# Performance work log

Measured on AMD Instinct MI355X. Metric: run time of the kernel, lower is better.

The kernel has to match this reference:

```python
import jax, jax.numpy as jnp
import numpy as np

B, S, D = 2, 2048, 1024
H, DH = 16, 64  # n_heads, d_head = d_model // n_heads


def setup_inputs() -> dict:
    key = jax.random.key(0)
    ks = jax.random.split(key, 12)
    scale = 1.0 / np.sqrt(D)
    return {
        "queries": jax.random.normal(ks[0], (B, S, D), jnp.float32),
        "keys": jax.random.normal(ks[1], (B, S, D), jnp.float32),
        "values": jax.random.normal(ks[2], (B, S, D), jnp.float32),
        "mask": jax.random.randint(ks[3], (1, 1, S, S), 0, 2, jnp.int32),
        "Wq": jax.random.normal(ks[4], (D, D), jnp.float32) * scale,
        "bq": jnp.zeros((D,), jnp.float32),
        "Wk": jax.random.normal(ks[5], (D, D), jnp.float32) * scale,
        "bk": jnp.zeros((D,), jnp.float32),
        "Wv": jax.random.normal(ks[6], (D, D), jnp.float32) * scale,
        "bv": jnp.zeros((D,), jnp.float32),
        "Wo": jax.random.normal(ks[7], (D, D), jnp.float32) * scale,
        "bo": jnp.zeros((D,), jnp.float32),
    }


def _split_proj(x):
    # (B, ?, H, DH) reshape then permute -> (B, H, ?, DH)
    b = x.shape[0]
    return x.reshape(b, -1, H, DH).transpose(0, 2, 1, 3)


def reference(queries, keys, values, mask, Wq, bq, Wk, bk, Wv, bv, Wo, bo):
    q = queries @ Wq.T + bq
    k = keys @ Wk.T + bk
    v = values @ Wv.T + bv
    # NOTE: original source applies split_proj to queries twice (faithful repro)
    q = _split_proj(_split_proj(q))
    k = _split_proj(k)
    v = _split_proj(v)
    scores = jnp.einsum('bhqd,bhkd->bhqk', q, k) / jnp.sqrt(jnp.float32(DH))
    scores = scores + mask.astype(scores.dtype) * (-1e9)
    attn = jax.nn.softmax(scores, axis=-1)
    out = jnp.einsum('bhqk,bhkd->bhqd', attn, v)  # (B,H,S,DH)
    out = out.transpose(0, 2, 1, 3).reshape(out.shape[0], -1, D)
    return out @ Wo.T + bo
```

## Files before the change

### kernel.cpp

```cpp
#include <hip/hip_runtime.h>
#include <hip/hip_bf16.h>
#include <cstddef>
#include <cstdint>


typedef __attribute__((ext_vector_type(8))) short bf16x8;
typedef __attribute__((ext_vector_type(4))) float f32x4;

__device__ __forceinline__ void gl_lds16(const void* g, void* l) {
    __builtin_amdgcn_global_load_lds(
        (const __attribute__((address_space(1))) void*)g,
        (__attribute__((address_space(3))) void*)l, 16, 0, 0);
}

__device__ __forceinline__ int4 cvt8(const float* __restrict__ src) {
    const float4 v0 = *(const float4*)src, v1 = *(const float4*)(src + 4);
    union { __hip_bfloat16 h[8]; int4 q; } u;
    u.h[0] = __float2bfloat16(v0.x); u.h[1] = __float2bfloat16(v0.y);
    u.h[2] = __float2bfloat16(v0.z); u.h[3] = __float2bfloat16(v0.w);
    u.h[4] = __float2bfloat16(v1.x); u.h[5] = __float2bfloat16(v1.y);
    u.h[6] = __float2bfloat16(v1.z); u.h[7] = __float2bfloat16(v1.w);
    return u.q;
}

__global__ __launch_bounds__(256) void prep(
    const float* __restrict__ q, const float* __restrict__ k, const float* __restrict__ v,
    const float* __restrict__ wq, const float* __restrict__ wk,
    const float* __restrict__ wv, const float* __restrict__ wo,
    const int* __restrict__ mask,
    __hip_bfloat16* __restrict__ dq, __hip_bfloat16* __restrict__ dk,
    __hip_bfloat16* __restrict__ dv, __hip_bfloat16* __restrict__ dwq,
    __hip_bfloat16* __restrict__ dwk, __hip_bfloat16* __restrict__ dwv,
    __hip_bfloat16* __restrict__ dwo,
    unsigned long long* __restrict__ mbits)
{
    const int bid = blockIdx.x;
    if (bid >= 8192) {
        const int wid  = ((bid - 8192) * 256 + threadIdx.x) >> 6;
        const int lane = threadIdx.x & 63;
        const int qr = wid >> 5, w64 = wid & 31;
        const int m = mask[(size_t)qr * 2048 + w64 * 64 + lane];
        const unsigned long long bal = __ballot(m != 0);
        if (lane == 0) mbits[(size_t)qr * 32 + w64] = bal;
        return;
    }
    const float* s; __hip_bfloat16* d; int base;
    if      (bid < 2048) { s = q;  d = dq;  base = bid; }
    else if (bid < 4096) { s = k;  d = dk;  base = bid - 2048; }
    else if (bid < 6144) { s = v;  d = dv;  base = bid - 4096; }
    else if (bid < 6656) { s = wq; d = dwq; base = bid - 6144; }
    else if (bid < 7168) { s = wk; d = dwk; base = bid - 6656; }
    else if (bid < 7680) { s = wv; d = dwv; base = bid - 7168; }
    else                 { s = wo; d = dwo; base = bid - 7680; }
    const size_t i = (size_t)base * 256 + threadIdx.x;
    *((int4*)d + i) = cvt8(s + i * 8);
}

template <int MR, typename OutT>
__device__ __forceinline__ void gemm_body(
    const __hip_bfloat16* __restrict__ A, const __hip_bfloat16* __restrict__ Bm,
    const float* __restrict__ bias, OutT* __restrict__ C,
    int N, int m0, int n0, int brow,
    __hip_bfloat16* As, __hip_bfloat16* Bs)
{
    const int t = threadIdx.x, lane = t & 63, w = t >> 6;
    const int l15 = lane & 15, g = lane >> 4;
    const int wr = w >> 1, wc = w & 1;
    constexpr int NI = MR / 32;

    f32x4 acc[NI][4] = {};

    for (int k0 = 0; k0 < 1024; k0 += 64) {
        __syncthreads();
        #pragma unroll
        for (int it = 0; it < NI; ++it) {
            const int c = it * 256 + t, row = c >> 3, c8 = c & 7;
            gl_lds16(A + (size_t)(m0 + row) * 1024 + k0 + c8 * 8, (char*)As + c * 16);
        }
        #pragma unroll
        for (int it = 0; it < 4; ++it) {
            const int c = it * 256 + t, row = c >> 3, c8 = c & 7;
            gl_lds16(Bm + (size_t)(n0 + row) * 1024 + k0 + c8 * 8, (char*)Bs + c * 16);
        }
        __syncthreads();
        #pragma unroll
        for (int kk = 0; kk < 64; kk += 32) {
            bf16x8 af[NI], bfr[4];
            #pragma unroll
            for (int i = 0; i < NI; ++i)
                af[i] = *(const bf16x8*)((const char*)As + (wr * (MR / 2) + i * 16 + l15) * 128 + kk * 2 + g * 16);
            #pragma unroll
            for (int j = 0; j < 4; ++j)
                bfr[j] = *(const bf16x8*)((const char*)Bs + (wc * 64 + j * 16 + l15) * 128 + kk * 2 + g * 16);
            #pragma unroll
            for (int i = 0; i < NI; ++i)
                #pragma unroll
                for (int j = 0; j < 4; ++j)
                    acc[i][j] = __builtin_amdgcn_mfma_f32_16x16x32_bf16(af[i], bfr[j], acc[i][j], 0, 0, 0);
        }
    }

    #pragma unroll
    for (int i = 0; i < NI; ++i) {
        const int m = m0 + wr * (MR / 2) + i * 16 + g * 4;
        #pragma unroll
        for (int j = 0; j < 4; ++j) {
            const int n = n0 + wc * 64 + j * 16 + l15;
            const float bc = brow ? 0.f : bias[n];
            #pragma unroll
            for (int r = 0; r < 4; ++r) {
                const float v = acc[i][j][r] + (brow ? bias[m + r] : bc);
                C[(size_t)(m + r) * N + n] = (OutT)v;
            }
        }
    }
}

__global__ __launch_bounds__(256) void qkv_gemm(
    const __hip_bfloat16* __restrict__ qin, const __hip_bfloat16* __restrict__ kin,
    const __hip_bfloat16* __restrict__ vin,
    const __hip_bfloat16* __restrict__ Wqb, const __hip_bfloat16* __restrict__ Wkb,
    const __hip_bfloat16* __restrict__ Wvb,
    const float* __restrict__ bq, const float* __restrict__ bk, const float* __restrict__ bv,
    __hip_bfloat16* __restrict__ qbuf, __hip_bfloat16* __restrict__ kbuf,
    __hip_bfloat16* __restrict__ vtb)
{
    __shared__ __align__(16) __hip_bfloat16 As[128 * 64];
    __shared__ __align__(16) __hip_bfloat16 Bs[128 * 64];
    const int z = blockIdx.z;
    if (z == 0)
        gemm_body<128>(qin, Wqb, bq, qbuf, 1024, blockIdx.y * 128, blockIdx.x * 128, 0, As, Bs);
    else if (z == 1)
        gemm_body<128>(kin, Wkb, bk, kbuf, 1024, blockIdx.y * 128, blockIdx.x * 128, 0, As, Bs);
    else
        gemm_body<128>(Wvb, vin, bv, vtb, 4096, blockIdx.x * 128, blockIdx.y * 128, 1, As, Bs);
}

__global__ __launch_bounds__(256) void out_gemm(
    const __hip_bfloat16* __restrict__ A, const __hip_bfloat16* __restrict__ Bm,
    const float* __restrict__ bias, float* __restrict__ C)
{
    __shared__ __align__(16) __hip_bfloat16 As[64 * 64];
    __shared__ __align__(16) __hip_bfloat16 Bs[128 * 64];
    gemm_body<64>(A, Bm, bias, C, 1024, blockIdx.y * 64, blockIdx.x * 128, 0, As, Bs);
}

__global__ __launch_bounds__(512, 4) void attn_mfma(
    const __hip_bfloat16* __restrict__ qb,
    const __hip_bfloat16* __restrict__ kb,
    const __hip_bfloat16* __restrict__ vt,
    const unsigned long long* __restrict__ mbits,
    __hip_bfloat16* __restrict__ ctx)
{
    __shared__ __align__(16) char smem[65536];

    const int t = threadIdx.x, lane = t & 63, w = t >> 6;
    const int grp = w >> 2, wl = w & 3;
    const int l15 = lane & 15, g = lane >> 4;
    const int tloc = t & 255;

    const int bid = blockIdx.x;
    const int xcd = bid & 7, ii = bid >> 3;
    const int bh = (xcd << 2) + (ii >> 4), qt = ii & 15;
    const int b = bh >> 4, a = bh & 15;
    const int q0 = qt * 128;
    const int kt0 = grp * 16;

    constexpr float SC_LOG2E = 0.18033688011112042f;
    constexpr float OFFC     = -17.312340490667561f;
    constexpr float MASKB    = -1.0e9f;

    bf16x8 qreg[2][2];
    int qgl[2];
    #pragma unroll
    for (int u = 0; u < 2; ++u) {
        const int qg = q0 + wl * 32 + u * 16 + l15;
        qgl[u] = qg;
        const int srow = (qg & 127) * 16 + a;
        #pragma unroll
        for (int half = 0; half < 2; ++half)
            qreg[u][half] = *(const bf16x8*)&qb[(size_t)(b * 2048 + srow) * 1024 + qt * 64 + (half * 4 + g) * 8];
    }

    const int srow0 = tloc >> 3, scc = tloc & 7;
    const int scs = scc ^ (srow0 & 7);
    const char* kSrc = (const char*)(kb + (size_t)(b * 2048 + kt0 * 64 + srow0) * 1024 + a * 64 + scs * 8);
    const char* vSrc = (const char*)(vt + (size_t)(a * 64 + srow0) * 4096 + b * 2048 + kt0 * 64 + scs * 8);
    char* kDst = smem + grp * 16384 + tloc * 16;
    char* vDst = smem + 32768 + grp * 16384 + tloc * 16;

    auto stage = [&](int bufn) {
        gl_lds16(kSrc,          kDst + bufn * 8192);
        gl_lds16(kSrc + 65536,  kDst + bufn * 8192 + 4096);
        gl_lds16(vSrc,          vDst + bufn * 8192);
        gl_lds16(vSrc + 262144, vDst + bufn * 8192 + 4096);
        kSrc += 131072;
        vSrc += 128;
    };

    int kofs[2][4], vofs[2][4];
    #pragma unroll
    for (int x = 0; x < 2; ++x)
        #pragma unroll
        for (int nf = 0; nf < 4; ++nf) {
            const int rr = nf * 16 + l15;
            const int sw = ((x * 4 + g) ^ (rr & 7)) << 4;
            kofs[x][nf] = grp * 16384 + rr * 128 + sw;
            vofs[x][nf] = 32768 + grp * 16384 + rr * 128 + sw;
        }

    const unsigned long long* mbP0 = mbits + (size_t)qgl[0] * 32 + kt0;
    const unsigned long long* mbP1 = mbits + (size_t)qgl[1] * 32 + kt0;

    bf16x8 ones;
    #pragma unroll
    for (int e = 0; e < 8; ++e) ones[e] = (short)0x3F80;

    f32x4 accd[2][4] = {};
    f32x4 accl[2] = {};

    stage(0);
    __syncthreads();

    auto do_tile = [&](int buf, bool doStage) {
        if (doStage) stage(buf ^ 1);
        const uint2 mw0 = *(const uint2*)mbP0; ++mbP0;
        const uint2 mw1 = *(const uint2*)mbP1; ++mbP1;

        f32x4 sf[2][4] = {};
        #pragma unroll
        for (int half = 0; half < 2; ++half)
            #pragma unroll
            for (int nf = 0; nf < 4; ++nf) {
                const bf16x8 kf = *(const bf16x8*)(smem + kofs[half][nf] + buf * 8192);
                sf[0][nf] = __builtin_amdgcn_mfma_f32_16x16x32_bf16(kf, qreg[0][half], sf[0][nf], 0, 0, 0);
                sf[1][nf] = __builtin_amdgcn_mfma_f32_16x16x32_bf16(kf, qreg[1][half], sf[1][nf], 0, 0, 0);
            }

        unsigned Wrd[2][4][2];
        #pragma unroll
        for (int u = 0; u < 2; ++u) {
            const uint2 mwv = u ? mw1 : mw0;
            #pragma unroll
            for (int nf = 0; nf < 4; ++nf) {
                const unsigned word = (nf & 2) ? mwv.y : mwv.x;
                const int bsh = ((nf & 1) << 4) + (g << 2);
                float pr[4];
                #pragma unroll
                for (int r = 0; r < 4; ++r) {
                    const bool msk = (word >> (bsh + r)) & 1u;
                    pr[r] = __builtin_amdgcn_exp2f(
                        fmaf(sf[u][nf][r], SC_LOG2E, msk ? MASKB : OFFC));
                }
                Wrd[u][nf][0] = __builtin_amdgcn_perm(
                    __float_as_uint(pr[1]) + 0x8000u,
                    __float_as_uint(pr[0]) + 0x8000u, 0x07060302u);
                Wrd[u][nf][1] = __builtin_amdgcn_perm(
                    __float_as_uint(pr[3]) + 0x8000u,
                    __float_as_uint(pr[2]) + 0x8000u, 0x07060302u);
            }
        }

        #pragma unroll
        for (int jj = 0; jj < 2; ++jj) {
            bf16x8 paf[2];
            #pragma unroll
            for (int u = 0; u < 2; ++u) {
                unsigned f0 = Wrd[u][2 * jj][0], f2 = Wrd[u][2 * jj + 1][0];
                unsigned f1 = Wrd[u][2 * jj][1], f3 = Wrd[u][2 * jj + 1][1];
                asm volatile("v_permlane32_swap_b32 %0, %1" : "+v"(f0), "+v"(f2));
                asm volatile("v_permlane16_swap_b32 %0, %1" : "+v"(f0), "+v"(f2));
                asm volatile("v_permlane32_swap_b32 %0, %1" : "+v"(f1), "+v"(f3));
                asm volatile("v_permlane16_swap_b32 %0, %1" : "+v"(f1), "+v"(f3));
                union { unsigned uw[4]; bf16x8 v; } uu;
                uu.uw[0] = f0; uu.uw[1] = f1; uu.uw[2] = f2; uu.uw[3] = f3;
                paf[u] = uu.v;
                accl[u] = __builtin_amdgcn_mfma_f32_16x16x32_bf16(paf[u], ones, accl[u], 0, 0, 0);
            }
            #pragma unroll
            for (int df = 0; df < 4; ++df) {
                const bf16x8 vf = *(const bf16x8*)(smem + vofs[jj][df] + buf * 8192);
                accd[0][df] = __builtin_amdgcn_mfma_f32_16x16x32_bf16(paf[0], vf, accd[0][df], 0, 0, 0);
                accd[1][df] = __builtin_amdgcn_mfma_f32_16x16x32_bf16(paf[1], vf, accd[1][df], 0, 0, 0);
            }
        }
        __syncthreads();
    };

    #pragma unroll 1
    for (int it2 = 0; it2 < 8; ++it2) {
        do_tile(0, true);
        do_tile(1, it2 != 7);
    }

    float* cmbO = (float*)smem;
    float* cmbL = (float*)(smem + 32768);
    if (grp == 0) {
        #pragma unroll
        for (int u = 0; u < 2; ++u)
            #pragma unroll
            for (int r = 0; r < 4; ++r) {
                const int row = wl * 32 + u * 16 + (g << 2) + r;
                #pragma unroll
                for (int df = 0; df < 4; ++df)
                    cmbO[row * 64 + df * 16 + l15] = accd[u][df][r];
                if (l15 == 0) cmbL[row] = accl[u][r];
            }
    }
    __syncthreads();
    if (grp == 1) {
        #pragma unroll
        for (int u = 0; u < 2; ++u)
            #pragma unroll
            for (int r = 0; r < 4; ++r) {
                const int row = wl * 32 + u * 16 + (g << 2) + r;
                const float lsum = accl[u][r] + cmbL[row];
                const float inv = 1.0f / lsum;
                const int qglob = q0 + row;
                #pragma unroll
                for (int df = 0; df < 4; ++df) {
                    const float o = accd[u][df][r] + cmbO[row * 64 + df * 16 + l15];
                    ctx[(size_t)(b * 2048 + qglob) * 1024 + (a << 6) + df * 16 + l15] =
                        __float2bfloat16(o * inv);
                }
            }
    }
}

extern "C" void kernel_launch(void* const* d_in, const int* in_sizes, int n_in,
                              void* d_out, int out_size, void* d_ws, size_t ws_size,
                              hipStream_t stream)
{
    const float* queries = (const float*)d_in[0];
    const float* keys    = (const float*)d_in[1];
    const float* values  = (const float*)d_in[2];
    const int*   mask    = (const int*)  d_in[3];
    const float* Wq = (const float*)d_in[4];
    const float* bq = (const float*)d_in[5];
    const float* Wk = (const float*)d_in[6];
    const float* bk = (const float*)d_in[7];
    const float* Wv = (const float*)d_in[8];
    const float* bv = (const float*)d_in[9];
    const float* Wo = (const float*)d_in[10];
    const float* bo = (const float*)d_in[11];

    const size_t NM = (size_t)4096 * 1024;
    const size_t NW = (size_t)1024 * 1024;
    __hip_bfloat16* p = (__hip_bfloat16*)d_ws;
    __hip_bfloat16* qin = p;  p += NM;
    __hip_bfloat16* kin = p;  p += NM;
    __hip_bfloat16* vin = p;  p += NM;
    __hip_bfloat16* Wqb = p;  p += NW;
    __hip_bfloat16* Wkb = p;  p += NW;
    __hip_bfloat16* Wvb = p;  p += NW;
    __hip_bfloat16* Wob = p;  p += NW;
    __hip_bfloat16* qbuf = p; p += NM;
    __hip_bfloat16* kbuf = p; p += NM;
    __hip_bfloat16* vtb  = p; p += NM;
    unsigned long long* mbits = (unsigned long long*)p;
    __hip_bfloat16* ctxb = qin;

    prep<<<dim3(24576), dim3(256), 0, stream>>>(
        queries, keys, values, Wq, Wk, Wv, Wo, mask,
        qin, kin, vin, Wqb, Wkb, Wvb, Wob, mbits);

    qkv_gemm<<<dim3(8, 32, 3), dim3(256), 0, stream>>>(
        qin, kin, vin, Wqb, Wkb, Wvb, bq, bk, bv, qbuf, kbuf, vtb);

    attn_mfma<<<dim3(512), dim3(512), 0, stream>>>(qbuf, kbuf, vtb, mbits, ctxb);

    out_gemm<<<dim3(8, 64), dim3(256), 0, stream>>>(ctxb, Wob, bo, (float*)d_out);
}
```

Baseline: 154.9 us.

## Halve attention key tile to 32 to cut LDS and double occupancy

Shrinks the attention kernel's per-stage K/V tile from 64 to 32 keys, with a new V swizzle and a 32-bit mask word per tile. Shared memory drops from 64KB to about 33KB, and launch bounds ask for 8 blocks per CU instead of 4. The aim is more resident waves to hide the global-to-LDS loads and the exp/MFMA latency. In exchange, the loop runs twice as many iterations, each with its own barrier, and does less MFMA work per sync.

After: 565.2 us. 265% more time.

```diff
diff --git a/kernel.cpp b/kernel.cpp
--- a/kernel.cpp
+++ b/kernel.cpp
@@ -145,14 +145,14 @@
     gemm_body<64>(A, Bm, bias, C, 1024, blockIdx.y * 64, blockIdx.x * 128, 0, As, Bs);
 }
 
-__global__ __launch_bounds__(512, 4) void attn_mfma(
+__global__ __launch_bounds__(512, 8) void attn_mfma(
     const __hip_bfloat16* __restrict__ qb,
     const __hip_bfloat16* __restrict__ kb,
     const __hip_bfloat16* __restrict__ vt,
     const unsigned long long* __restrict__ mbits,
     __hip_bfloat16* __restrict__ ctx)
 {
-    __shared__ __align__(16) char smem[65536];
+    __shared__ __align__(16) char smem[33280];
 
     const int t = threadIdx.x, lane = t & 63, w = t >> 6;
     const int grp = w >> 2, wl = w & 3;
@@ -164,7 +164,7 @@
     const int bh = (xcd << 2) + (ii >> 4), qt = ii & 15;
     const int b = bh >> 4, a = bh & 15;
     const int q0 = qt * 128;
-    const int kt0 = grp * 16;
+    const int kt0 = grp * 32;
 
     constexpr float SC_LOG2E = 0.18033688011112042f;
     constexpr float OFFC     = -17.312340490667561f;
@@ -182,35 +182,39 @@
             qreg[u][half] = *(const bf16x8*)&qb[(size_t)(b * 2048 + srow) * 1024 + qt * 64 + (half * 4 + g) * 8];
     }
 
-    const int srow0 = tloc >> 3, scc = tloc & 7;
-    const int scs = scc ^ (srow0 & 7);
-    const char* kSrc = (const char*)(kb + (size_t)(b * 2048 + kt0 * 64 + srow0) * 1024 + a * 64 + scs * 8);
-    const char* vSrc = (const char*)(vt + (size_t)(a * 64 + srow0) * 4096 + b * 2048 + kt0 * 64 + scs * 8);
-    char* kDst = smem + grp * 16384 + tloc * 16;
-    char* vDst = smem + 32768 + grp * 16384 + tloc * 16;
+    const int krow0 = tloc >> 3, kcc = tloc & 7;
+    const int kcs = kcc ^ (krow0 & 7);
+    const int vrow0 = tloc >> 2, vcc = tloc & 3;
+    const int vcs = vcc ^ ((vrow0 >> 1) & 3);
+    const char* kSrc = (const char*)(kb + (size_t)(b * 2048 + kt0 * 32 + krow0) * 1024 + a * 64 + kcs * 8);
+    const char* vSrc = (const char*)(vt + (size_t)(a * 64 + vrow0) * 4096 + b * 2048 + kt0 * 32 + vcs * 8);
+    char* kDst = smem + grp * 8192 + tloc * 16;
+    char* vDst = smem + 16384 + grp * 8192 + tloc * 16;
 
     auto stage = [&](int bufn) {
-        gl_lds16(kSrc,          kDst + bufn * 8192);
-        gl_lds16(kSrc + 65536,  kDst + bufn * 8192 + 4096);
-        gl_lds16(vSrc,          vDst + bufn * 8192);
-        gl_lds16(vSrc + 262144, vDst + bufn * 8192 + 4096);
-        kSrc += 131072;
-        vSrc += 128;
+        gl_lds16(kSrc, kDst + bufn * 4096);
+        gl_lds16(vSrc, vDst + bufn * 4096);
+        kSrc += 65536;
+        vSrc += 64;
     };
 
-    int kofs[2][4], vofs[2][4];
+    int kofs[2][2], vofs[4];
     #pragma unroll
     for (int x = 0; x < 2; ++x)
         #pragma unroll
-        for (int nf = 0; nf < 4; ++nf) {
+        for (int nf = 0; nf < 2; ++nf) {
             const int rr = nf * 16 + l15;
-            const int sw = ((x * 4 + g) ^ (rr & 7)) << 4;
-            kofs[x][nf] = grp * 16384 + rr * 128 + sw;
-            vofs[x][nf] = 32768 + grp * 16384 + rr * 128 + sw;
-        }
-
-    const unsigned long long* mbP0 = mbits + (size_t)qgl[0] * 32 + kt0;
-    const unsigned long long* mbP1 = mbits + (size_t)qgl[1] * 32 + kt0;
+            kofs[x][nf] = grp * 8192 + rr * 128 + (((x * 4 + g) ^ (rr & 7)) << 4);
+        }
+    #pragma unroll
+    for (int df = 0; df < 4; ++df) {
+        const int rr = df * 16 + l15;
+        vofs[df] = 16384 + grp * 8192 + rr * 64 + ((g ^ ((rr >> 1) & 3)) << 4);
+    }
+
+    const unsigned* mbU = (const unsigned*)mbits;
+    const unsigned* mbP0 = mbU + (size_t)qgl[0] * 64 + kt0;
+    const unsigned* mbP1 = mbU + (size_t)qgl[1] * 64 + kt0;
 
     bf16x8 ones;
     #pragma unroll
@@ -224,27 +228,26 @@
 
     auto do_tile = [&](int buf, bool doStage) {
         if (doStage) stage(buf ^ 1);
-        const uint2 mw0 = *(const uint2*)mbP0; ++mbP0;
-        const uint2 mw1 = *(const uint2*)mbP1; ++mbP1;
-
-        f32x4 sf[2][4] = {};
+        const unsigned mw0 = *mbP0; ++mbP0;
+        const unsigned mw1 = *mbP1; ++mbP1;
+
+        f32x4 sf[2][2] = {};
         #pragma unroll
         for (int half = 0; half < 2; ++half)
             #pragma unroll
-            for (int nf = 0; nf < 4; ++nf) {
-                const bf16x8 kf = *(const bf16x8*)(smem + kofs[half][nf] + buf * 8192);
+            for (int nf = 0; nf < 2; ++nf) {
+                const bf16x8 kf = *(const bf16x8*)(smem + kofs[half][nf] + buf * 4096);
                 sf[0][nf] = __builtin_amdgcn_mfma_f32_16x16x32_bf16(kf, qreg[0][half], sf[0][nf], 0, 0, 0);
                 sf[1][nf] = __builtin_amdgcn_mfma_f32_16x16x32_bf16(kf, qreg[1][half], sf[1][nf], 0, 0, 0);
             }
 
-        unsigned Wrd[2][4][2];
+        unsigned Wrd[2][2][2];
         #pragma unroll
         for (int u = 0; u < 2; ++u) {
-            const uint2 mwv = u ? mw1 : mw0;
-            #pragma unroll
-            for (int nf = 0; nf < 4; ++nf) {
-                const unsigned word = (nf & 2) ? mwv.y : mwv.x;
-                const int bsh = ((nf & 1) << 4) + (g << 2);
+            const unsigned word = u ? mw1 : mw0;
+            #pragma unroll
+            for (int nf = 0; nf < 2; ++nf) {
+                const int bsh = (nf << 4) + (g << 2);
                 float pr[4];
                 #pragma unroll
                 for (int r = 0; r < 4; ++r) {
@@ -261,13 +264,12 @@
             }
         }
 
-        #pragma unroll
-        for (int jj = 0; jj < 2; ++jj) {
+        {
             bf16x8 paf[2];
             #pragma unroll
             for (int u = 0; u < 2; ++u) {
-                unsigned f0 = Wrd[u][2 * jj][0], f2 = Wrd[u][2 * jj + 1][0];
-                unsigned f1 = Wrd[u][2 * jj][1], f3 = Wrd[u][2 * jj + 1][1];
+                unsigned f0 = Wrd[u][0][0], f2 = Wrd[u][1][0];
+                unsigned f1 = Wrd[u][0][1], f3 = Wrd[u][1][1];
                 asm volatile("v_permlane32_swap_b32 %0, %1" : "+v"(f0), "+v"(f2));
                 asm volatile("v_permlane16_swap_b32 %0, %1" : "+v"(f0), "+v"(f2));
                 asm volatile("v_permlane32_swap_b32 %0, %1" : "+v"(f1), "+v"(f3));
@@ -279,7 +281,7 @@
             }
             #pragma unroll
             for (int df = 0; df < 4; ++df) {
-                const bf16x8 vf = *(const bf16x8*)(smem + vofs[jj][df] + buf * 8192);
+                const bf16x8 vf = *(const bf16x8*)(smem + vofs[df] + buf * 4096);
                 accd[0][df] = __builtin_amdgcn_mfma_f32_16x16x32_bf16(paf[0], vf, accd[0][df], 0, 0, 0);
                 accd[1][df] = __builtin_amdgcn_mfma_f32_16x16x32_bf16(paf[1], vf, accd[1][df], 0, 0, 0);
             }
@@ -288,9 +290,9 @@
     };
 
     #pragma unroll 1
-    for (int it2 = 0; it2 < 8; ++it2) {
+    for (int it2 = 0; it2 < 16; ++it2) {
         do_tile(0, true);
-        do_tile(1, it2 != 7);
+        do_tile(1, it2 != 15);
     }
 
     float* cmbO = (float*)smem;
```
